# Performance work log

Hardware: AMD Instinct MI355X
Metric: run time of the kernel (lower is better)

## Reference

```python
import jax, jax.numpy as jnp
import numpy as np

C = 256      # d_model
H = 8        # nhead
DF = 1024    # dim_feedforward
LE = 2048    # ego tokens
LA = 2048    # other-agent tokens
N_MATCH = 1024


def setup_inputs() -> dict:
    key = jax.random.key(0)
    ks = jax.random.split(key, 16)
    def rn(k, shape, s=0.02):
        return jax.random.normal(k, shape, dtype=jnp.float32) * s
    inp = {}
    inp['x_ego'] = jax.random.normal(ks[0], (LE, C), dtype=jnp.float32)
    inp['x_agent'] = jax.random.normal(ks[1], (LA, C), dtype=jnp.float32)
    # query_fusion MLP(2C -> C -> C -> C), torch Linear weight is (out, in)
    inp['Wf1'] = rn(ks[2], (C, 2 * C)); inp['bf1'] = jnp.zeros((C,), jnp.float32)
    inp['Wf2'] = rn(ks[3], (C, C));     inp['bf2'] = jnp.zeros((C,), jnp.float32)
    inp['Wf3'] = rn(ks[4], (C, C));     inp['bf3'] = jnp.zeros((C,), jnp.float32)
    # nn.MultiheadAttention packed in-proj and out-proj
    inp['Wqkv'] = rn(ks[5], (3 * C, C)); inp['bqkv'] = jnp.zeros((3 * C,), jnp.float32)
    inp['Wo'] = rn(ks[6], (C, C));       inp['bo'] = jnp.zeros((C,), jnp.float32)
    # FFN
    inp['W1'] = rn(ks[7], (DF, C)); inp['b1'] = jnp.zeros((DF,), jnp.float32)
    inp['W2'] = rn(ks[8], (C, DF)); inp['b2'] = jnp.zeros((C,), jnp.float32)
    # LayerNorms
    inp['g1'] = jnp.ones((C,), jnp.float32); inp['be1'] = jnp.zeros((C,), jnp.float32)
    inp['g2'] = jnp.ones((C,), jnp.float32); inp['be2'] = jnp.zeros((C,), jnp.float32)
    # unique 1D positions: first N_MATCH agent positions overlap ego, rest don't
    inp['pos_ego'] = jnp.arange(LE, dtype=jnp.int32)
    pa = np.concatenate([np.arange(N_MATCH), np.arange(LA - N_MATCH) + 10_000_000])
    inp['pos_agent'] = jnp.asarray(pa, dtype=jnp.int32)
    inp['n_remain'] = LA - N_MATCH  # static python int
    return inp


def _ln(t, g, b):
    m = t.mean(-1, keepdims=True)
    v = t.var(-1, keepdims=True)
    return (t - m) / jnp.sqrt(v + 1e-5) * g + b


def reference(x_ego, x_agent, Wf1, bf1, Wf2, bf2, Wf3, bf3, Wqkv, bqkv, Wo, bo,
              W1, b1, W2, b2, g1, be1, g2, be2, pos_ego, pos_agent, n_remain):
    # ---- position-keyed grouping / fuse (replaces the host-side dict loop) ----
    eq = pos_agent[:, None] == pos_ego[None, :]          # [La, Le]
    matched_e = eq.any(axis=0)                           # ego token has same-pos agent token
    agent_for_ego = jnp.argmax(eq, axis=0)               # [Le] matching agent index (valid where matched)
    fused_in = jnp.concatenate([x_ego, x_agent[agent_for_ego]], axis=-1)  # [Le, 2C]
    h = jax.nn.relu(fused_in @ Wf1.T + bf1)
    h = jax.nn.relu(h @ Wf2.T + bf2)
    fused = h @ Wf3.T + bf3                              # query_fusion MLP output [Le, C]
    ego_out = jnp.where(matched_e[:, None], fused, x_ego)
    # agent tokens with no ego match, in original agent order (fixed count n_remain)
    remain_idx = jnp.nonzero(~eq.any(axis=1), size=n_remain)[0]
    q = jnp.concatenate([ego_out, x_agent[remain_idx]], axis=0)[None]  # (1, Lq, C)
    kv = jnp.concatenate([x_ego, x_agent], axis=0)[None]               # (1, Lk, C)
    # ---- MultiheadAttention (batch_first, eval: dropout off) ----
    Wq, Wk, Wv = jnp.split(Wqkv, 3, axis=0)
    bq, bk, bv = jnp.split(bqkv, 3, axis=0)
    dh = C // H
    def heads(t, W, b):
        return (t @ W.T + b).reshape(1, -1, H, dh).transpose(0, 2, 1, 3)
    qh, kh, vh = heads(q, Wq, bq), heads(kv, Wk, bk), heads(kv, Wv, bv)
    scores = jnp.einsum('bhqd,bhkd->bhqk', qh, kh) / (float(dh) ** 0.5)
    attn = jax.nn.softmax(scores, axis=-1)
    o = jnp.einsum('bhqk,bhkd->bhqd', attn, vh).transpose(0, 2, 1, 3).reshape(1, -1, C)
    o = o @ Wo.T + bo
    # ---- residual + norm1 + FFN + residual + norm2 ----
    yq = _ln(q + o, g1, be1)
    ff = jax.nn.relu(yq @ W1.T + b1) @ W2.T + b2
    return _ln(yq + ff, g2, be2)
```

## Files before the change

kernel.cpp:

```cpp
#include <hip/hip_runtime.h>


#define LE 2048
#define LA 2048
#define CDIM 256
#define HN 8
#define DH 32
#define DFF 1024
#define NREM 1024
#define LQC 3072
#define LKC 4096
#define KSPLIT 8
#define NIT (LKC / KSPLIT / 64)

typedef unsigned short u16;
typedef unsigned int u32;
typedef __attribute__((ext_vector_type(8))) short bf16x8;
typedef __attribute__((ext_vector_type(8))) _Float16 f16x8;
typedef __attribute__((ext_vector_type(4))) float f32x4;

#define MFMA __builtin_amdgcn_mfma_f32_16x16x32_bf16

__device__ __forceinline__ u32 pk_bf16(float a, float b) {
    u32 ua = (__builtin_bit_cast(u32, a) + 0x8000u) >> 16;
    u32 ub = (__builtin_bit_cast(u32, b) + 0x8000u) >> 16;
    return ua | (ub << 16);
}
__device__ __forceinline__ u16 bf16_1(float a) {
    return (u16)((__builtin_bit_cast(u32, a) + 0x8000u) >> 16);
}
__device__ __forceinline__ float fast_exp2(float x) {
    return __builtin_amdgcn_exp2f(x);
}
__device__ __forceinline__ bf16x8 ld_pack8(const float* p) {
    float4 f0 = *(const float4*)p;
    float4 f1 = *(const float4*)(p + 4);
    union { u32 u[4]; bf16x8 v; } o;
    o.u[0] = pk_bf16(f0.x, f0.y); o.u[1] = pk_bf16(f0.z, f0.w);
    o.u[2] = pk_bf16(f1.x, f1.y); o.u[3] = pk_bf16(f1.z, f1.w);
    return o.v;
}

struct WPtrs { const float* p[7]; };
__constant__ __device__ const int woff[8] = {0, 131072, 196608, 262144,
                                             458752, 524288, 786432, 1048576};

__global__ __launch_bounds__(1024) void k_prep(const int* __restrict__ pos_ego,
                                               const int* __restrict__ pos_agent,
                                               int* __restrict__ afe,
                                               int* __restrict__ matched,
                                               int* __restrict__ remain,
                                               const float* __restrict__ x_ego,
                                               const float* __restrict__ x_agent,
                                               WPtrs wp, u16* __restrict__ wb,
                                               u16* __restrict__ kv_b) {
    const int b = blockIdx.x;
    const int t = threadIdx.x;
    if (b == 0) {
        __shared__ int keyA[4096], valA[4096], keyE[4096];
        __shared__ int unm[2048];
#pragma unroll
        for (int i = 0; i < 4; ++i) { keyA[t + i * 1024] = -1; keyE[t + i * 1024] = -1; }
        __syncthreads();
#pragma unroll
        for (int i = 0; i < 2; ++i) {
            int a = t + i * 1024;
            int p = pos_agent[a];
            u32 h = ((u32)p * 2654435761u) >> 20;
            while (true) {
                int prev = atomicCAS(&keyA[h], -1, p);
                if (prev == -1) { valA[h] = a; break; }
                h = (h + 1) & 4095;
            }
            int e = t + i * 1024;
            int pe = pos_ego[e];
            u32 he = ((u32)pe * 2654435761u) >> 20;
            while (true) {
                int prev = atomicCAS(&keyE[he], -1, pe);
                if (prev == -1) break;
                he = (he + 1) & 4095;
            }
        }
        __syncthreads();
#pragma unroll
        for (int i = 0; i < 2; ++i) {
            int e = t + i * 1024;
            int p = pos_ego[e];
            u32 h = ((u32)p * 2654435761u) >> 20;
            int idx = 0, fnd = 0;
            while (true) {
                int k = keyA[h];
                if (k == p) { idx = valA[h]; fnd = 1; break; }
                if (k == -1) break;
                h = (h + 1) & 4095;
            }
            afe[e] = idx;
            matched[e] = fnd;
            int a = t + i * 1024;
            int pa_ = pos_agent[a];
            u32 ha = ((u32)pa_ * 2654435761u) >> 20;
            int fnd2 = 0;
            while (true) {
                int k = keyE[ha];
                if (k == pa_) { fnd2 = 1; break; }
                if (k == -1) break;
                ha = (ha + 1) & 4095;
            }
            unm[a] = !fnd2;
        }
        __syncthreads();
        int f0 = unm[2 * t], f1 = unm[2 * t + 1];
        int cnt = f0 + f1;
        valA[t] = cnt;
        __syncthreads();
        for (int off = 1; off < 1024; off <<= 1) {
            int v = (t >= off) ? valA[t - off] : 0;
            __syncthreads();
            valA[t] += v;
            __syncthreads();
        }
        int pos = valA[t] - cnt;
        if (f0 && pos < NREM) remain[pos] = 2 * t;
        if (f1 && pos + f0 < NREM) remain[pos + f0] = 2 * t + 1;
    } else if (b <= 128) {
        int g = ((b - 1) * 1024 + t) * 8;
        int s = 0;
#pragma unroll
        for (int i = 1; i < 7; ++i) s += (g >= woff[i]);
        const float* src = wp.p[s] + (g - woff[s]);
        float4 f0 = *(const float4*)(src);
        float4 f1 = *(const float4*)(src + 4);
        uint4 o;
        o.x = pk_bf16(f0.x, f0.y); o.y = pk_bf16(f0.z, f0.w);
        o.z = pk_bf16(f1.x, f1.y); o.w = pk_bf16(f1.z, f1.w);
        *(uint4*)(wb + g) = o;
    } else {
        int tt = (b - 129) * 1024 + t;
        int j = tt >> 5, c8 = tt & 31;
        const float* src = (j < LE) ? (x_ego + (size_t)j * CDIM)
                                    : (x_agent + (size_t)(j - LE) * CDIM);
        float4 f0 = *(const float4*)(src + c8 * 8);
        float4 f1 = *(const float4*)(src + c8 * 8 + 4);
        uint4 o;
        o.x = pk_bf16(f0.x, f0.y); o.y = pk_bf16(f0.z, f0.w);
        o.z = pk_bf16(f1.x, f1.y); o.w = pk_bf16(f1.z, f1.w);
        *(uint4*)(kv_b + (size_t)j * CDIM + c8 * 8) = o;
    }
}

__global__ __launch_bounds__(256) void k_fmlp(const float* __restrict__ x_ego,
                                              const float* __restrict__ x_agent,
                                              const int* __restrict__ afe,
                                              const int* __restrict__ matched,
                                              const int* __restrict__ remain,
                                              const u16* __restrict__ Wf1_b,
                                              const u16* __restrict__ Wf2_b,
                                              const u16* __restrict__ Wf3_b,
                                              const float* __restrict__ bf1,
                                              const float* __restrict__ bf2,
                                              const float* __restrict__ bf3,
                                              float* __restrict__ qbuf,
                                              u16* __restrict__ qbuf_b) {
    const int blk = blockIdx.x;
    const int tid = threadIdx.x;
    if (blk >= 128) {
        int rb = (blk - 128) * 64 + (tid >> 2);
        int row = LE + rb;
        int col = (tid & 3) * 64;
        int idx = remain[rb];
        idx = min(max(idx, 0), LA - 1);
        const float* src = x_agent + (size_t)idx * CDIM + col;
        float* dq = qbuf + (size_t)row * CDIM + col;
        u16* db = qbuf_b + (size_t)row * CDIM + col;
#pragma unroll
        for (int i = 0; i < 16; ++i) {
            float4 v = *(const float4*)(src + i * 4);
            *(float4*)(dq + i * 4) = v;
            *(uint2*)(db + i * 4) = make_uint2(pk_bf16(v.x, v.y), pk_bf16(v.z, v.w));
        }
        return;
    }
    __shared__ u16 h1[16 * 256];
    __shared__ u16 h2[16 * 256];
    const int w = tid >> 6, lane = tid & 63, quad = lane >> 4, qi = lane & 15;
    const int R0 = blk * 16;
    const int rg = R0 + qi;
    {
        const float* pe = x_ego + (size_t)rg * CDIM + quad * 8;
        const float* pg = x_agent + (size_t)afe[rg] * CDIM + quad * 8;
        f32x4 acc[4] = {};
        const u16* pb = Wf1_b + (size_t)(w * 64 + qi) * 512 + quad * 8;
#pragma unroll
        for (int kk = 0; kk < 256; kk += 32) {
            bf16x8 a = ld_pack8(pe + kk);
#pragma unroll
            for (int j = 0; j < 4; ++j) {
                bf16x8 bfr = *(const bf16x8*)(pb + (size_t)j * 16 * 512 + kk);
                acc[j] = MFMA(a, bfr, acc[j], 0, 0, 0);
            }
        }
#pragma unroll
        for (int kk = 0; kk < 256; kk += 32) {
            bf16x8 a = ld_pack8(pg + kk);
#pragma unroll
            for (int j = 0; j < 4; ++j) {
                bf16x8 bfr = *(const bf16x8*)(pb + (size_t)j * 16 * 512 + 256 + kk);
                acc[j] = MFMA(a, bfr, acc[j], 0, 0, 0);
            }
        }
#pragma unroll
        for (int j = 0; j < 4; ++j) {
            int col = w * 64 + j * 16 + qi;
            float bs = bf1[col];
#pragma unroll
            for (int r = 0; r < 4; ++r) {
                int row = quad * 4 + r;
                float v = fmaxf(acc[j][r] + bs, 0.f);
                int byte = (row * 512 + col * 2) ^ ((row & 7) << 4);
                *(u16*)((char*)h1 + byte) = bf16_1(v);
            }
        }
    }
    __syncthreads();
    {
        f32x4 acc[4] = {};
        const u16* pb = Wf2_b + (size_t)(w * 64 + qi) * 256 + quad * 8;
#pragma unroll
        for (int kk = 0; kk < 256; kk += 32) {
            int byte = (qi * 512 + (kk + quad * 8) * 2) ^ ((qi & 7) << 4);
            bf16x8 a = *(const bf16x8*)((char*)h1 + byte);
#pragma unroll
            for (int j = 0; j < 4; ++j) {
                bf16x8 bfr = *(const bf16x8*)(pb + (size_t)j * 16 * 256 + kk);
                acc[j] = MFMA(a, bfr, acc[j], 0, 0, 0);
            }
        }
#pragma unroll
        for (int j = 0; j < 4; ++j) {
            int col = w * 64 + j * 16 + qi;
            float bs = bf2[col];
#pragma unroll
            for (int r = 0; r < 4; ++r) {
                int row = quad * 4 + r;
                float v = fmaxf(acc[j][r] + bs, 0.f);
                int byte = (row * 512 + col * 2) ^ ((row & 7) << 4);
                *(u16*)((char*)h2 + byte) = bf16_1(v);
            }
        }
    }
    __syncthreads();
    {
        f32x4 acc[4] = {};
        const u16* pb = Wf3_b + (size_t)(w * 64 + qi) * 256 + quad * 8;
#pragma unroll
        for (int kk = 0; kk < 256; kk += 32) {
            int byte = (qi * 512 + (kk + quad * 8) * 2) ^ ((qi & 7) << 4);
            bf16x8 a = *(const bf16x8*)((char*)h2 + byte);
#pragma unroll
            for (int j = 0; j < 4; ++j) {
                bf16x8 bfr = *(const bf16x8*)(pb + (size_t)j * 16 * 256 + kk);
                acc[j] = MFMA(a, bfr, acc[j], 0, 0, 0);
            }
        }
        int m[4];
#pragma unroll
        for (int r = 0; r < 4; ++r) m[r] = matched[R0 + quad * 4 + r];
#pragma unroll
        for (int j = 0; j < 4; ++j) {
            int col = w * 64 + j * 16 + qi;
            float bs = bf3[col];
#pragma unroll
            for (int r = 0; r < 4; ++r) {
                int row = R0 + quad * 4 + r;
                float v = acc[j][r] + bs;
                if (!m[r]) v = x_ego[(size_t)row * CDIM + col];
                qbuf[(size_t)row * CDIM + col] = v;
                qbuf_b[(size_t)row * CDIM + col] = bf16_1(v);
            }
        }
    }
}

__global__ __launch_bounds__(256) void k_qkv(const u16* __restrict__ qbuf_b,
                                             const u16* __restrict__ kv_b,
                                             const u16* __restrict__ Wq,
                                             const u16* __restrict__ Wkv,
                                             const float* __restrict__ bqkv,
                                             u16* __restrict__ qb,
                                             u16* __restrict__ kbp,
                                             u16* __restrict__ vtb,
                                             float qscale) {
    int b;
    {
        int p = blockIdx.x;
        int c = p & 7, s = p >> 3;
        b = c * 88 + s;
    }
    const u16 *A, *B;
    const float* bias;
    int bm, bn, mode;
    if (b < 192) {
        A = qbuf_b; B = Wq; bias = bqkv;
        bm = (b >> 2) * 64; bn = (b & 3) * 64; mode = 0;
    } else {
        int c = b - 192;
        A = kv_b; B = Wkv; bias = bqkv + 256;
        bm = (c >> 3) * 64; bn = (c & 7) * 64; mode = 1;
    }
    const int tid = threadIdx.x;
    const int w = tid >> 6, lane = tid & 63;
    const int quad = lane >> 4, qi = lane & 15;
    const int wm = w >> 1, wn = w & 1;
    const int K = 256;

    const u16* pa0 = A + (size_t)(bm + wm * 32 + qi) * K + quad * 8;
    const u16* pa1 = pa0 + (size_t)16 * K;
    const u16* pb0 = B + (size_t)(bn + wn * 32 + qi) * K + quad * 8;
    const u16* pb1 = pb0 + (size_t)16 * K;

    f32x4 acc00 = {0.f, 0.f, 0.f, 0.f}, acc01 = {0.f, 0.f, 0.f, 0.f};
    f32x4 acc10 = {0.f, 0.f, 0.f, 0.f}, acc11 = {0.f, 0.f, 0.f, 0.f};
#pragma unroll 4
    for (int k = 0; k < 256; k += 32) {
        bf16x8 a0 = *(const bf16x8*)(pa0 + k);
        bf16x8 a1 = *(const bf16x8*)(pa1 + k);
        bf16x8 b0 = *(const bf16x8*)(pb0 + k);
        bf16x8 b1 = *(const bf16x8*)(pb1 + k);
        acc00 = MFMA(a0, b0, acc00, 0, 0, 0);
        acc01 = MFMA(a0, b1, acc01, 0, 0, 0);
        acc10 = MFMA(a1, b0, acc10, 0, 0, 0);
        acc11 = MFMA(a1, b1, acc11, 0, 0, 0);
    }
#pragma unroll
    for (int i = 0; i < 2; ++i) {
#pragma unroll
        for (int j = 0; j < 2; ++j) {
            f32x4 acc = (i == 0) ? (j == 0 ? acc00 : acc01) : (j == 0 ? acc10 : acc11);
            int n = bn + wn * 32 + j * 16 + qi;
            int mbase = bm + wm * 32 + i * 16 + quad * 4;
            float bs = bias[n];
            float v[4];
#pragma unroll
            for (int r = 0; r < 4; ++r) v[r] = acc[r] + bs;
            if (mode == 0) {
#pragma unroll
                for (int r = 0; r < 4; ++r)
                    qb[(size_t)(mbase + r) * 256 + n] = bf16_1(v[r] * qscale);
            } else if (n < 256) {
#pragma unroll
                for (int r = 0; r < 4; ++r)
                    kbp[(size_t)(mbase + r) * 256 + n] = bf16_1(v[r]);
            } else {
                ushort4 o4;
                o4.x = bf16_1(v[0]); o4.y = bf16_1(v[1]);
                o4.z = bf16_1(v[2]); o4.w = bf16_1(v[3]);
                *(ushort4*)(vtb + (size_t)(n - 256) * LKC + mbase) = o4;
            }
        }
    }
}

__global__ __launch_bounds__(256) void attn_mfma(const u16* __restrict__ qb,
                                                 const u16* __restrict__ kb,
                                                 const u16* __restrict__ vtb,
                                                 float* __restrict__ Pl,
                                                 u16* __restrict__ Pacc) {
    __shared__ u16 Kt[2][64 * 32];
    __shared__ u16 Vt[2][32 * 64];
    __shared__ u16 plds[4][16 * 64];
    const int tid = threadIdx.x;
    const int w = tid >> 6, lane = tid & 63;
    const int quad = lane >> 4, qi = lane & 15;
    int h, ks, q0;
    {
        int p = (blockIdx.z * gridDim.y + blockIdx.y) * gridDim.x + blockIdx.x;
        int c = p & 7, s = p >> 3;
        int l = c * 384 + s;
        int qblk = l % 48;
        int hk = l / 48;
        h = hk & 7; ks = hk >> 3;
        q0 = qblk * 64 + w * 16;
    }

    bf16x8 qf = *(const bf16x8*)(qb + (size_t)(q0 + qi) * CDIM + h * DH + quad * 8);

    f32x4 O0 = {0.f, 0.f, 0.f, 0.f}, O1 = {0.f, 0.f, 0.f, 0.f};
    float lsum = 0.f;

    const int krow = w * 16 + (lane >> 2), kcp = lane & 3;
    const int kc = kcp ^ (krow & 3);
    const u16* kg0 = kb + (size_t)krow * CDIM + h * DH + kc * 8;
    const int kdst = krow * 32 + kcp * 8;
    const int vd = w * 8 + (lane >> 3), vcp = lane & 7;
    const int vc = vcp ^ (vd & 7);
    const u16* vg0 = vtb + (size_t)(h * DH + vd) * LKC + vc * 8;
    const int vdst = vd * 64 + vcp * 8;

    const int ka0 = qi * 32 + ((quad ^ (qi & 3)) << 3);
    const int v00o = qi * 64 + ((quad ^ (qi & 7)) << 3);
    const int v01o = qi * 64 + (((quad + 4) ^ (qi & 7)) << 3);
    const int swz = (qi & 7);
    const int rd0 = qi * 64 + ((quad ^ swz) << 3);
    const int rd1 = qi * 64 + (((4 + quad) ^ swz) << 3);
    const int half = (quad & 1) << 2;

    int kt = ks * (LKC / KSPLIT);
    {
        bf16x8 kr = *(const bf16x8*)(kg0 + (size_t)kt * CDIM);
        bf16x8 vr = *(const bf16x8*)(vg0 + kt);
        *(bf16x8*)&Kt[0][kdst] = kr;
        *(bf16x8*)&Vt[0][vdst] = vr;
    }
    int buf = 0;
    for (int it = 0; it < NIT; ++it, kt += 64) {
        __syncthreads();
        bf16x8 knext, vnext;
        const bool more = (it + 1 < NIT);
        if (more) {
            knext = *(const bf16x8*)(kg0 + (size_t)(kt + 64) * CDIM);
            vnext = *(const bf16x8*)(vg0 + kt + 64);
        }

        bf16x8 a0 = *(const bf16x8*)&Kt[buf][ka0];
        bf16x8 a1 = *(const bf16x8*)&Kt[buf][ka0 + 16 * 32];
        bf16x8 a2 = *(const bf16x8*)&Kt[buf][ka0 + 32 * 32];
        bf16x8 a3 = *(const bf16x8*)&Kt[buf][ka0 + 48 * 32];
        f32x4 z = {0.f, 0.f, 0.f, 0.f};
        f32x4 s0 = MFMA(a0, qf, z, 0, 0, 0);
        f32x4 s1 = MFMA(a1, qf, z, 0, 0, 0);
        f32x4 s2 = MFMA(a2, qf, z, 0, 0, 0);
        f32x4 s3 = MFMA(a3, qf, z, 0, 0, 0);

        float p0[4], p1[4], p2[4], p3[4];
#pragma unroll
        for (int r = 0; r < 4; ++r) {
            p0[r] = fast_exp2(s0[r]); p1[r] = fast_exp2(s1[r]);
            p2[r] = fast_exp2(s2[r]); p3[r] = fast_exp2(s3[r]);
            lsum += p0[r] + p1[r] + p2[r] + p3[r];
        }

        u16* pb = &plds[w][0];
#pragma unroll
        for (int t2 = 0; t2 < 4; ++t2) {
            int jg = t2 * 2 + (quad >> 1);
            int off = qi * 64 + ((jg ^ swz) << 3) + half;
            uint2 pw;
            float* pp = (t2 == 0) ? p0 : (t2 == 1) ? p1 : (t2 == 2) ? p2 : p3;
            pw.x = pk_bf16(pp[0], pp[1]);
            pw.y = pk_bf16(pp[2], pp[3]);
            *(uint2*)&pb[off] = pw;
        }
        bf16x8 pa0 = *(bf16x8*)&pb[rd0];
        bf16x8 pa1 = *(bf16x8*)&pb[rd1];

        bf16x8 v00 = *(const bf16x8*)&Vt[buf][v00o];
        bf16x8 v01 = *(const bf16x8*)&Vt[buf][v01o];
        bf16x8 v10 = *(const bf16x8*)&Vt[buf][v00o + 16 * 64];
        bf16x8 v11 = *(const bf16x8*)&Vt[buf][v01o + 16 * 64];
        O0 = MFMA(pa0, v00, O0, 0, 0, 0);
        O0 = MFMA(pa1, v01, O0, 0, 0, 0);
        O1 = MFMA(pa0, v10, O1, 0, 0, 0);
        O1 = MFMA(pa1, v11, O1, 0, 0, 0);

        if (more) {
            *(bf16x8*)&Kt[buf ^ 1][kdst] = knext;
            *(bf16x8*)&Vt[buf ^ 1][vdst] = vnext;
        }
        buf ^= 1;
    }

    lsum += __shfl_xor(lsum, 16, 64);
    lsum += __shfl_xor(lsum, 32, 64);

    int pbase = (h * KSPLIT + ks) * LQC + q0;
    if (quad == 0) Pl[pbase + qi] = lsum;
#pragma unroll
    for (int r = 0; r < 4; ++r) {
        int q = quad * 4 + r;
        u16* pa = Pacc + (size_t)(pbase + q) * 32;
        pa[qi] = __builtin_bit_cast(u16, (_Float16)O0[r]);
        pa[16 + qi] = __builtin_bit_cast(u16, (_Float16)O1[r]);
    }
}

__global__ __launch_bounds__(256) void k_oln(const float* __restrict__ Pl,
                                             const u16* __restrict__ Pacc,
                                             const u16* __restrict__ Wo_b,
                                             const float* __restrict__ bo,
                                             const float* __restrict__ qbuf,
                                             const float* __restrict__ g1,
                                             const float* __restrict__ be1,
                                             float* __restrict__ yq,
                                             u16* __restrict__ yq_b) {
    __shared__ u16 At[16 * 256];
    __shared__ float red[16][4][2];
    const int tid = threadIdx.x;
    const int R0 = blockIdx.x * 16;
    {
        int row = tid >> 4, cg = tid & 15;
        int h = cg >> 1, dh = (cg & 1) * 16;
        int r = R0 + row;
        float L = 0.f;
        float o[16] = {};
#pragma unroll
        for (int ks = 0; ks < 8; ++ks) {
            size_t pidx = (size_t)(h * 8 + ks) * LQC + r;
            L += Pl[pidx];
            const u16* pa = Pacc + pidx * 32 + dh;
            f16x8 v0 = *(const f16x8*)(pa);
            f16x8 v1 = *(const f16x8*)(pa + 8);
#pragma unroll
            for (int i = 0; i < 8; ++i) {
                o[i] += (float)v0[i];
                o[8 + i] += (float)v1[i];
            }
        }
        float invL = 1.0f / L;
        int cb = h * 32 + dh;
#pragma unroll
        for (int i = 0; i < 8; ++i) {
            int c0 = cb + 2 * i;
            u32 pk = pk_bf16(o[2 * i] * invL, o[2 * i + 1] * invL);
            int byte = (row * 512 + c0 * 2) ^ ((row & 7) << 4);
            *(u32*)((char*)At + byte) = pk;
        }
    }
    __syncthreads();
    const int w = tid >> 6, lane = tid & 63, quad = lane >> 4, qi = lane & 15;
    f32x4 acc[4] = {};
    const u16* pb = Wo_b + (size_t)(w * 64 + qi) * 256 + quad * 8;
#pragma unroll
    for (int kk = 0; kk < 256; kk += 32) {
        int byte = (qi * 512 + (kk + quad * 8) * 2) ^ ((qi & 7) << 4);
        bf16x8 a = *(const bf16x8*)((char*)At + byte);
#pragma unroll
        for (int j = 0; j < 4; ++j) {
            bf16x8 bfr = *(const bf16x8*)(pb + (size_t)j * 16 * 256 + kk);
            acc[j] = MFMA(a, bfr, acc[j], 0, 0, 0);
        }
    }
    float v[4][4], s[4] = {}, sq[4] = {};
#pragma unroll
    for (int j = 0; j < 4; ++j) {
        int col = w * 64 + j * 16 + qi;
        float bs = bo[col];
#pragma unroll
        for (int r = 0; r < 4; ++r) {
            int row = R0 + quad * 4 + r;
            float x = acc[j][r] + bs + qbuf[(size_t)row * CDIM + col];
            v[j][r] = x; s[r] += x; sq[r] += x * x;
        }
    }
#pragma unroll
    for (int off = 1; off < 16; off <<= 1) {
#pragma unroll
        for (int r = 0; r < 4; ++r) {
            s[r] += __shfl_xor(s[r], off, 64);
            sq[r] += __shfl_xor(sq[r], off, 64);
        }
    }
    if (qi == 0) {
#pragma unroll
        for (int r = 0; r < 4; ++r) {
            red[quad * 4 + r][w][0] = s[r];
            red[quad * 4 + r][w][1] = sq[r];
        }
    }
    __syncthreads();
    float mean[4], rstd[4];
#pragma unroll
    for (int r = 0; r < 4; ++r) {
        int rl = quad * 4 + r;
        float st = red[rl][0][0] + red[rl][1][0] + red[rl][2][0] + red[rl][3][0];
        float sqt = red[rl][0][1] + red[rl][1][1] + red[rl][2][1] + red[rl][3][1];
        mean[r] = st * (1.f / 256.f);
        float var = sqt * (1.f / 256.f) - mean[r] * mean[r];
        rstd[r] = rsqrtf(var + 1e-5f);
    }
#pragma unroll
    for (int j = 0; j < 4; ++j) {
        int col = w * 64 + j * 16 + qi;
        float gg = g1[col], bb = be1[col];
#pragma unroll
        for (int r = 0; r < 4; ++r) {
            int row = R0 + quad * 4 + r;
            float o = (v[j][r] - mean[r]) * rstd[r] * gg + bb;
            yq[(size_t)row * CDIM + col] = o;
            yq_b[(size_t)row * CDIM + col] = bf16_1(o);
        }
    }
}

__global__ __launch_bounds__(256) void k_ffn(const u16* __restrict__ yq_b,
                                             const float* __restrict__ yq,
                                             const u16* __restrict__ W1_b,
                                             const float* __restrict__ b1,
                                             const u16* __restrict__ W2_b,
                                             const float* __restrict__ b2,
                                             const float* __restrict__ g2,
                                             const float* __restrict__ be2,
                                             float* __restrict__ out) {
    __shared__ u16 hT[16 * 1024];
    __shared__ float red[16][4][2];
    const int tid = threadIdx.x;
    const int w = tid >> 6, lane = tid & 63, quad = lane >> 4, qi = lane & 15;
    const int R0 = blockIdx.x * 16;
    {
        const u16* pa = yq_b + (size_t)(R0 + qi) * 256 + quad * 8;
        f32x4 acc[16] = {};
        const u16* pb = W1_b + (size_t)(w * 256 + qi) * 256 + quad * 8;
#pragma unroll
        for (int kk = 0; kk < 256; kk += 32) {
            bf16x8 a = *(const bf16x8*)(pa + kk);
#pragma unroll
            for (int j = 0; j < 16; ++j) {
                bf16x8 bfr = *(const bf16x8*)(pb + (size_t)j * 16 * 256 + kk);
                acc[j] = MFMA(a, bfr, acc[j], 0, 0, 0);
            }
        }
#pragma unroll
        for (int j = 0; j < 16; ++j) {
            int col = w * 256 + j * 16 + qi;
            float bs = b1[col];
#pragma unroll
            for (int r = 0; r < 4; ++r) {
                int row = quad * 4 + r;
                float v = fmaxf(acc[j][r] + bs, 0.f);
                int byte = (row * 2048 + col * 2) ^ ((row & 7) << 4);
                *(u16*)((char*)hT + byte) = bf16_1(v);
            }
        }
    }
    __syncthreads();
    f32x4 acc[4] = {};
    const u16* pb = W2_b + (size_t)(w * 64 + qi) * 1024 + quad * 8;
#pragma unroll 4
    for (int kk = 0; kk < 1024; kk += 32) {
        int byte = (qi * 2048 + (kk + quad * 8) * 2) ^ ((qi & 7) << 4);
        bf16x8 a = *(const bf16x8*)((char*)hT + byte);
#pragma unroll
        for (int j = 0; j < 4; ++j) {
            bf16x8 bfr = *(const bf16x8*)(pb + (size_t)j * 16 * 1024 + kk);
            acc[j] = MFMA(a, bfr, acc[j], 0, 0, 0);
        }
    }
    float v[4][4], s[4] = {}, sq[4] = {};
#pragma unroll
    for (int j = 0; j < 4; ++j) {
        int col = w * 64 + j * 16 + qi;
        float bs = b2[col];
#pragma unroll
        for (int r = 0; r < 4; ++r) {
            int row = R0 + quad * 4 + r;
            float x = acc[j][r] + bs + yq[(size_t)row * CDIM + col];
            v[j][r] = x; s[r] += x; sq[r] += x * x;
        }
    }
#pragma unroll
    for (int off = 1; off < 16; off <<= 1) {
#pragma unroll
        for (int r = 0; r < 4; ++r) {
            s[r] += __shfl_xor(s[r], off, 64);
            sq[r] += __shfl_xor(sq[r], off, 64);
        }
    }
    if (qi == 0) {
#pragma unroll
        for (int r = 0; r < 4; ++r) {
            red[quad * 4 + r][w][0] = s[r];
            red[quad * 4 + r][w][1] = sq[r];
        }
    }
    __syncthreads();
    float mean[4], rstd[4];
#pragma unroll
    for (int r = 0; r < 4; ++r) {
        int rl = quad * 4 + r;
        float st = red[rl][0][0] + red[rl][1][0] + red[rl][2][0] + red[rl][3][0];
        float sqt = red[rl][0][1] + red[rl][1][1] + red[rl][2][1] + red[rl][3][1];
        mean[r] = st * (1.f / 256.f);
        float var = sqt * (1.f / 256.f) - mean[r] * mean[r];
        rstd[r] = rsqrtf(var + 1e-5f);
    }
#pragma unroll
    for (int j = 0; j < 4; ++j) {
        int col = w * 64 + j * 16 + qi;
        float gg = g2[col], bb = be2[col];
#pragma unroll
        for (int r = 0; r < 4; ++r) {
            int row = R0 + quad * 4 + r;
            out[(size_t)row * CDIM + col] = (v[j][r] - mean[r]) * rstd[r] * gg + bb;
        }
    }
}

extern "C" void kernel_launch(void* const* d_in, const int* in_sizes, int n_in,
                              void* d_out, int out_size, void* d_ws, size_t ws_size,
                              hipStream_t stream) {
    const float* x_ego = (const float*)d_in[0];
    const float* x_agent = (const float*)d_in[1];
    const float* Wf1 = (const float*)d_in[2];
    const float* bf1 = (const float*)d_in[3];
    const float* Wf2 = (const float*)d_in[4];
    const float* bf2 = (const float*)d_in[5];
    const float* Wf3 = (const float*)d_in[6];
    const float* bf3 = (const float*)d_in[7];
    const float* Wqkv = (const float*)d_in[8];
    const float* bqkv = (const float*)d_in[9];
    const float* Wo = (const float*)d_in[10];
    const float* bo = (const float*)d_in[11];
    const float* W1 = (const float*)d_in[12];
    const float* b1 = (const float*)d_in[13];
    const float* W2 = (const float*)d_in[14];
    const float* b2 = (const float*)d_in[15];
    const float* g1 = (const float*)d_in[16];
    const float* be1 = (const float*)d_in[17];
    const float* g2 = (const float*)d_in[18];
    const float* be2 = (const float*)d_in[19];
    const int* pos_ego = (const int*)d_in[20];
    const int* pos_agent = (const int*)d_in[21];

    float* ws = (float*)d_ws;
    size_t o = 0;
    float* qbuf = ws + o; o += 786432;
    float* yq = ws + o; o += 786432;
    float* Pl = ws + o; o += HN * KSPLIT * LQC;
    u16* Pacc = (u16*)(ws + o); o += (size_t)HN * KSPLIT * LQC * 16;
    u16* wb = (u16*)(ws + o); o += 524288;
    u16* qbuf_b = (u16*)(ws + o); o += 393216;
    u16* kv_b = (u16*)(ws + o); o += 524288;
    u16* qb = (u16*)(ws + o); o += 393216;
    u16* kb = (u16*)(ws + o); o += 524288;
    u16* vtb = (u16*)(ws + o); o += 524288;
    u16* yq_b = (u16*)(ws + o); o += 393216;
    int* afe = (int*)(ws + o);
    int* matched = afe + LE;
    int* remain = matched + LE;

    const u16* Wf1_b = wb + 0;
    const u16* Wf2_b = wb + 131072;
    const u16* Wf3_b = wb + 196608;
    const u16* Wq_b = wb + 262144;
    const u16* Wkv_b = wb + 327680;
    const u16* Wo_b = wb + 458752;
    const u16* W1_b = wb + 524288;
    const u16* W2_b = wb + 786432;

    WPtrs wp;
    wp.p[0] = Wf1; wp.p[1] = Wf2; wp.p[2] = Wf3; wp.p[3] = Wqkv;
    wp.p[4] = Wo; wp.p[5] = W1; wp.p[6] = W2;

    k_prep<<<257, 1024, 0, stream>>>(pos_ego, pos_agent, afe, matched, remain,
                                     x_ego, x_agent, wp, wb, kv_b);

    const float qscale = 0.17677669529663687f * 1.4426950408889634f;

    k_fmlp<<<144, 256, 0, stream>>>(x_ego, x_agent, afe, matched, remain,
                                    Wf1_b, Wf2_b, Wf3_b, bf1, bf2, bf3,
                                    qbuf, qbuf_b);

    k_qkv<<<704, 256, 0, stream>>>(qbuf_b, kv_b, Wq_b, Wkv_b, bqkv, qb, kb, vtb, qscale);

    attn_mfma<<<dim3(LQC / 64, HN, KSPLIT), 256, 0, stream>>>(qb, kb, vtb, Pl, Pacc);

    k_oln<<<LQC / 16, 256, 0, stream>>>(Pl, Pacc, Wo_b, bo, qbuf, g1, be1, yq, yq_b);

    k_ffn<<<LQC / 16, 256, 0, stream>>>(yq_b, yq, W1_b, b1, W2_b, b2, g2, be2,
                                        (float*)d_out);
}
```

Baseline: 223.0 us.

## Split FFN into tiled GEMM plus fused GEMM-LayerNorm and halve attention K-split

The fused FFN kernel, which computed the hidden layer in shared memory per 16-row block, is replaced by a separate 64x64-tiled bf16 MFMA GEMM with ReLU that writes the hidden activations to global memory. A second kernel with 512 threads then does the W2 GEMM, residual and LayerNorm. The attention split-K factor drops from 8 to 4, reducing partial-result traffic and the reduction work in the output-projection kernel at the cost of fewer attention blocks. The change trades an extra global round trip of the 3072x1024 hidden tensor for better parallelism and less redundant W1 loading.

```diff
diff --git a/kernel.cpp b/kernel.cpp
--- a/kernel.cpp
+++ b/kernel.cpp
@@ -10,7 +10,7 @@
 #define NREM 1024
 #define LQC 3072
 #define LKC 4096
-#define KSPLIT 8
+#define KSPLIT 4
 #define NIT (LKC / KSPLIT / 64)
 
 typedef unsigned short u16;
@@ -39,6 +39,16 @@
     o.u[0] = pk_bf16(f0.x, f0.y); o.u[1] = pk_bf16(f0.z, f0.w);
     o.u[2] = pk_bf16(f1.x, f1.y); o.u[3] = pk_bf16(f1.z, f1.w);
     return o.v;
+}
+
+__device__ __forceinline__ void xcd_tile(int& bm, int& bn) {
+    int gx = gridDim.x;
+    int tot = gx * gridDim.y;
+    int p = blockIdx.y * gx + blockIdx.x;
+    int l = p;
+    if (!(tot & 7)) { int c = p & 7, s = p >> 3; l = c * (tot >> 3) + s; }
+    bm = (l / gx) * 64;
+    bn = (l % gx) * 64;
 }
 
 struct WPtrs { const float* p[7]; };
@@ -281,6 +291,67 @@
     }
 }
 
+template <int EPI, bool RELU>
+__global__ __launch_bounds__(256) void gemm_bf16(const u16* __restrict__ A,
+                                                 const u16* __restrict__ B,
+                                                 const float* __restrict__ bias,
+                                                 void* __restrict__ C,
+                                                 int M, int N, int K) {
+    const int tid = threadIdx.x;
+    const int w = tid >> 6, lane = tid & 63;
+    const int quad = lane >> 4, qi = lane & 15;
+    const int wm = w >> 1, wn = w & 1;
+    int bm, bn;
+    xcd_tile(bm, bn);
+
+    const u16* pa0 = A + (size_t)(bm + wm * 32 + qi) * K + quad * 8;
+    const u16* pa1 = pa0 + (size_t)16 * K;
+    const u16* pb0 = B + (size_t)(bn + wn * 32 + qi) * K + quad * 8;
+    const u16* pb1 = pb0 + (size_t)16 * K;
+
+    f32x4 acc00 = {0.f, 0.f, 0.f, 0.f}, acc01 = {0.f, 0.f, 0.f, 0.f};
+    f32x4 acc10 = {0.f, 0.f, 0.f, 0.f}, acc11 = {0.f, 0.f, 0.f, 0.f};
+
+#pragma unroll 4
+    for (int k = 0; k < K; k += 32) {
+        bf16x8 a0 = *(const bf16x8*)(pa0 + k);
+        bf16x8 a1 = *(const bf16x8*)(pa1 + k);
+        bf16x8 b0 = *(const bf16x8*)(pb0 + k);
+        bf16x8 b1 = *(const bf16x8*)(pb1 + k);
+        acc00 = MFMA(a0, b0, acc00, 0, 0, 0);
+        acc01 = MFMA(a0, b1, acc01, 0, 0, 0);
+        acc10 = MFMA(a1, b0, acc10, 0, 0, 0);
+        acc11 = MFMA(a1, b1, acc11, 0, 0, 0);
+    }
+
+#pragma unroll
+    for (int i = 0; i < 2; ++i) {
+#pragma unroll
+        for (int j = 0; j < 2; ++j) {
+            f32x4 acc = (i == 0) ? (j == 0 ? acc00 : acc01) : (j == 0 ? acc10 : acc11);
+            int n = bn + wn * 32 + j * 16 + qi;
+            int mbase = bm + wm * 32 + i * 16 + quad * 4;
+            float bs = bias[n];
+            float v[4];
+#pragma unroll
+            for (int r = 0; r < 4; ++r) {
+                float x = acc[r] + bs;
+                if (RELU) x = fmaxf(x, 0.f);
+                v[r] = x;
+            }
+            if (EPI == 0) {
+                float* Cf = (float*)C;
+#pragma unroll
+                for (int r = 0; r < 4; ++r) Cf[(size_t)(mbase + r) * N + n] = v[r];
+            } else {
+                u16* Cb = (u16*)C;
+#pragma unroll
+                for (int r = 0; r < 4; ++r) Cb[(size_t)(mbase + r) * N + n] = bf16_1(v[r]);
+            }
+        }
+    }
+}
+
 __global__ __launch_bounds__(256) void k_qkv(const u16* __restrict__ qbuf_b,
                                              const u16* __restrict__ kv_b,
                                              const u16* __restrict__ Wq,
@@ -375,7 +446,7 @@
     {
         int p = (blockIdx.z * gridDim.y + blockIdx.y) * gridDim.x + blockIdx.x;
         int c = p & 7, s = p >> 3;
-        int l = c * 384 + s;
+        int l = c * 192 + s;
         int qblk = l % 48;
         int hk = l / 48;
         h = hk & 7; ks = hk >> 3;
@@ -503,8 +574,8 @@
         float L = 0.f;
         float o[16] = {};
 #pragma unroll
-        for (int ks = 0; ks < 8; ++ks) {
-            size_t pidx = (size_t)(h * 8 + ks) * LQC + r;
+        for (int ks = 0; ks < KSPLIT; ++ks) {
+            size_t pidx = (size_t)(h * KSPLIT + ks) * LQC + r;
             L += Pl[pidx];
             const u16* pa = Pacc + pidx * 32 + dh;
             f16x8 v0 = *(const f16x8*)(pa);
@@ -591,100 +662,69 @@
     }
 }
 
-__global__ __launch_bounds__(256) void k_ffn(const u16* __restrict__ yq_b,
-                                             const float* __restrict__ yq,
-                                             const u16* __restrict__ W1_b,
-                                             const float* __restrict__ b1,
-                                             const u16* __restrict__ W2_b,
-                                             const float* __restrict__ b2,
-                                             const float* __restrict__ g2,
-                                             const float* __restrict__ be2,
-                                             float* __restrict__ out) {
-    __shared__ u16 hT[16 * 1024];
-    __shared__ float red[16][4][2];
+__global__ __launch_bounds__(512) void k_ffn2ln(const u16* __restrict__ ff1_b,
+                                                const float* __restrict__ yq,
+                                                const u16* __restrict__ W2_b,
+                                                const float* __restrict__ b2,
+                                                const float* __restrict__ g2,
+                                                const float* __restrict__ be2,
+                                                float* __restrict__ out) {
+    __shared__ float red[16][8][2];
     const int tid = threadIdx.x;
     const int w = tid >> 6, lane = tid & 63, quad = lane >> 4, qi = lane & 15;
     const int R0 = blockIdx.x * 16;
-    {
-        const u16* pa = yq_b + (size_t)(R0 + qi) * 256 + quad * 8;
-        f32x4 acc[16] = {};
-        const u16* pb = W1_b + (size_t)(w * 256 + qi) * 256 + quad * 8;
-#pragma unroll
-        for (int kk = 0; kk < 256; kk += 32) {
-            bf16x8 a = *(const bf16x8*)(pa + kk);
-#pragma unroll
-            for (int j = 0; j < 16; ++j) {
-                bf16x8 bfr = *(const bf16x8*)(pb + (size_t)j * 16 * 256 + kk);
-                acc[j] = MFMA(a, bfr, acc[j], 0, 0, 0);
-            }
-        }
-#pragma unroll
-        for (int j = 0; j < 16; ++j) {
-            int col = w * 256 + j * 16 + qi;
-            float bs = b1[col];
-#pragma unroll
-            for (int r = 0; r < 4; ++r) {
-                int row = quad * 4 + r;
-                float v = fmaxf(acc[j][r] + bs, 0.f);
-                int byte = (row * 2048 + col * 2) ^ ((row & 7) << 4);
-                *(u16*)((char*)hT + byte) = bf16_1(v);
-            }
-        }
-    }
-    __syncthreads();
-    f32x4 acc[4] = {};
-    const u16* pb = W2_b + (size_t)(w * 64 + qi) * 1024 + quad * 8;
-#pragma unroll 4
-    for (int kk = 0; kk < 1024; kk += 32) {
-        int byte = (qi * 2048 + (kk + quad * 8) * 2) ^ ((qi & 7) << 4);
-        bf16x8 a = *(const bf16x8*)((char*)hT + byte);
-#pragma unroll
-        for (int j = 0; j < 4; ++j) {
-            bf16x8 bfr = *(const bf16x8*)(pb + (size_t)j * 16 * 1024 + kk);
-            acc[j] = MFMA(a, bfr, acc[j], 0, 0, 0);
-        }
-    }
-    float v[4][4], s[4] = {}, sq[4] = {};
-#pragma unroll
-    for (int j = 0; j < 4; ++j) {
-        int col = w * 64 + j * 16 + qi;
+    const u16* pa = ff1_b + (size_t)(R0 + qi) * DFF + quad * 8;
+    const u16* pb0 = W2_b + (size_t)(w * 32 + qi) * DFF + quad * 8;
+    const u16* pb1 = pb0 + (size_t)16 * DFF;
+    f32x4 acc0 = {0.f, 0.f, 0.f, 0.f}, acc1 = {0.f, 0.f, 0.f, 0.f};
+#pragma unroll 8
+    for (int kk = 0; kk < DFF; kk += 32) {
+        bf16x8 a = *(const bf16x8*)(pa + kk);
+        acc0 = MFMA(a, *(const bf16x8*)(pb0 + kk), acc0, 0, 0, 0);
+        acc1 = MFMA(a, *(const bf16x8*)(pb1 + kk), acc1, 0, 0, 0);
+    }
+    float v[2][4], s[4], sq[4];
+#pragma unroll
+    for (int j = 0; j < 2; ++j) {
+        int col = w * 32 + j * 16 + qi;
         float bs = b2[col];
 #pragma unroll
         for (int r = 0; r < 4; ++r) {
             int row = R0 + quad * 4 + r;
-            float x = acc[j][r] + bs + yq[(size_t)row * CDIM + col];
-            v[j][r] = x; s[r] += x; sq[r] += x * x;
-        }
-    }
-#pragma unroll
-    for (int off = 1; off < 16; off <<= 1) {
+            float x = (j ? acc1[r] : acc0[r]) + bs + yq[(size_t)row * CDIM + col];
+            v[j][r] = x;
+            if (j == 0) { s[r] = x; sq[r] = x * x; }
+            else { s[r] += x; sq[r] += x * x; }
+        }
+    }
+#pragma unroll
+    for (int off = 1; off < 16; off <<= 1)
 #pragma unroll
         for (int r = 0; r < 4; ++r) {
             s[r] += __shfl_xor(s[r], off, 64);
             sq[r] += __shfl_xor(sq[r], off, 64);
         }
-    }
-    if (qi == 0) {
+    if (qi == 0)
 #pragma unroll
         for (int r = 0; r < 4; ++r) {
             red[quad * 4 + r][w][0] = s[r];
             red[quad * 4 + r][w][1] = sq[r];
         }
-    }
     __syncthreads();
     float mean[4], rstd[4];
 #pragma unroll
     for (int r = 0; r < 4; ++r) {
         int rl = quad * 4 + r;
-        float st = red[rl][0][0] + red[rl][1][0] + red[rl][2][0] + red[rl][3][0];
-        float sqt = red[rl][0][1] + red[rl][1][1] + red[rl][2][1] + red[rl][3][1];
+        float st = 0.f, sqt = 0.f;
+#pragma unroll
+        for (int ww = 0; ww < 8; ++ww) { st += red[rl][ww][0]; sqt += red[rl][ww][1]; }
         mean[r] = st * (1.f / 256.f);
         float var = sqt * (1.f / 256.f) - mean[r] * mean[r];
         rstd[r] = rsqrtf(var + 1e-5f);
     }
 #pragma unroll
-    for (int j = 0; j < 4; ++j) {
-        int col = w * 64 + j * 16 + qi;
+    for (int j = 0; j < 2; ++j) {
+        int col = w * 32 + j * 16 + qi;
         float gg = g2[col], bb = be2[col];
 #pragma unroll
         for (int r = 0; r < 4; ++r) {
@@ -733,6 +773,7 @@
     u16* kb = (u16*)(ws + o); o += 524288;
     u16* vtb = (u16*)(ws + o); o += 524288;
     u16* yq_b = (u16*)(ws + o); o += 393216;
+    u16* ff1_b = (u16*)(ws + o); o += 1572864;
     int* afe = (int*)(ws + o);
     int* matched = afe + LE;
     int* remain = matched + LE;
@@ -765,6 +806,8 @@
 
     k_oln<<<LQC / 16, 256, 0, stream>>>(Pl, Pacc, Wo_b, bo, qbuf, g1, be1, yq, yq_b);
 
-    k_ffn<<<LQC / 16, 256, 0, stream>>>(yq_b, yq, W1_b, b1, W2_b, b2, g2, be2,
-                                        (float*)d_out);
-}
+    gemm_bf16<1, true><<<dim3(16, 48), 256, 0, stream>>>(yq_b, W1_b, b1, ff1_b,
+                                                         LQC, DFF, 256);
+    k_ffn2ln<<<LQC / 16, 512, 0, stream>>>(ff1_b, yq, W2_b, b2, g2, be2,
+                                           (float*)d_out);
+}
```

Result: faster. 217.8 us (-2.3%).
